# Performance work log

Measured on AMD Instinct MI355X. Metric: run time of the kernel, lower is better.

## Reference

```python
import jax, jax.numpy as jnp
import numpy as np

V, S, D, H, L = 32000, 2048, 768, 12, 6
HD = D // H
EPS = 1e-5


def _sinusoidal_pe(s, d):
    pos = np.arange(s)[:, None].astype(np.float32)
    div = np.exp(np.arange(0, d, 2).astype(np.float32) * (-np.log(10000.0) / d))
    pe = np.zeros((s, d), dtype=np.float32)
    pe[:, 0::2] = np.sin(pos * div)
    pe[:, 1::2] = np.cos(pos * div)
    return jnp.asarray(pe)


def setup_inputs() -> dict:
    key = jax.random.key(0)
    ks = jax.random.split(key, 16)
    std = 0.02
    tok_emb = jax.random.normal(ks[0], (V, D), jnp.float32) * std
    tok_emb = tok_emb.at[1].set(0.0)  # padding_idx=1
    pos_enc = _sinusoidal_pe(S, D)
    attn_w = jax.random.normal(ks[1], (L, 3 * D, D), jnp.float32) * std
    attn_b = jnp.zeros((L, 3 * D), jnp.float32)
    proj_std = 0.02 / np.sqrt(2 * 6)
    proj_w = jax.random.normal(ks[2], (L, D, D), jnp.float32) * proj_std
    proj_b = jnp.zeros((L, D), jnp.float32)
    ln1_g = jnp.ones((L, D), jnp.float32); ln1_b = jnp.zeros((L, D), jnp.float32)
    ln2_g = jnp.ones((L, D), jnp.float32); ln2_b = jnp.zeros((L, D), jnp.float32)
    fc1_w = jax.random.normal(ks[3], (L, 4 * D, D), jnp.float32) * std
    fc1_b = jnp.zeros((L, 4 * D), jnp.float32)
    fc2_w = jax.random.normal(ks[4], (L, D, 4 * D), jnp.float32) * std
    fc2_b = jnp.zeros((L, D), jnp.float32)
    dec_w = jax.random.normal(ks[5], (V, D), jnp.float32) * std
    idx = jax.random.randint(ks[6], (2, S), 0, V)
    return dict(idx=idx, tok_emb=tok_emb, pos_enc=pos_enc, attn_w=attn_w,
                attn_b=attn_b, proj_w=proj_w, proj_b=proj_b, ln1_g=ln1_g,
                ln1_b=ln1_b, ln2_g=ln2_g, ln2_b=ln2_b, fc1_w=fc1_w,
                fc1_b=fc1_b, fc2_w=fc2_w, fc2_b=fc2_b, dec_w=dec_w)


def _ln(x, g, b):
    mu = jnp.mean(x, -1, keepdims=True)
    var = jnp.mean(jnp.square(x - mu), -1, keepdims=True)
    return (x - mu) * jax.lax.rsqrt(var + EPS) * g + b


def _forward(idx, tok_emb, pos_enc, attn_w, attn_b, proj_w, proj_b,
             ln1_g, ln1_b, ln2_g, ln2_b, fc1_w, fc1_b, fc2_w, fc2_b, dec_w):
    b, s = idx.shape
    x = tok_emb[idx] + pos_enc[:s]  # [b,s,d]
    for l in range(L):
        h = _ln(x, ln1_g[l], ln1_b[l])
        qkv = h @ attn_w[l].T + attn_b[l]
        q, k, v = jnp.split(qkv, 3, axis=-1)
        q = q.reshape(b, s, H, HD).transpose(0, 2, 1, 3)
        k = k.reshape(b, s, H, HD).transpose(0, 2, 1, 3)
        v = v.reshape(b, s, H, HD).transpose(0, 2, 1, 3)
        att = jnp.einsum('bhqd,bhkd->bhqk', q, k) * (1.0 / np.sqrt(HD))
        att = jax.nn.softmax(att, axis=-1)  # no causal mask in source
        y = jnp.einsum('bhqk,bhkd->bhqd', att, v)
        y = y.transpose(0, 2, 1, 3).reshape(b, s, D)
        x = x + (y @ proj_w[l].T + proj_b[l])
        h = _ln(x, ln2_g[l], ln2_b[l])
        h = jax.nn.gelu(h @ fc1_w[l].T + fc1_b[l])
        x = x + (h @ fc2_w[l].T + fc2_b[l])
    return x @ dec_w.T  # [b,s,V]


def reference(idx, tok_emb, pos_enc, attn_w, attn_b, proj_w, proj_b,
              ln1_g, ln1_b, ln2_g, ln2_b, fc1_w, fc1_b, fc2_w, fc2_b, dec_w):
    return _forward(idx, tok_emb, pos_enc, attn_w, attn_b, proj_w, proj_b,
                    ln1_g, ln1_b, ln2_g, ln2_b, fc1_w, fc1_b, fc2_w, fc2_b, dec_w)
```

## Files before the change

### kernel.cpp

```cpp
#include <hip/hip_runtime.h>
#include <hip/hip_bf16.h>
#include <stdint.h>


typedef unsigned short u16;
typedef __attribute__((ext_vector_type(8))) __bf16 bf16x8;
typedef __attribute__((ext_vector_type(4))) float f32x4;
typedef __attribute__((ext_vector_type(4))) unsigned int u32x4;
typedef __attribute__((ext_vector_type(4))) unsigned short u16x4;
typedef __attribute__((ext_vector_type(8))) unsigned short u16x8;

#define MFMA16(a, b, c) __builtin_amdgcn_mfma_f32_16x16x32_bf16((a), (b), (c), 0, 0, 0)

__device__ __forceinline__ float b2f(u16 u) {
  union { unsigned int i; float f; } x; x.i = ((unsigned int)u) << 16; return x.f;
}
__device__ __forceinline__ u16 f2b(float f) {
  union { float f; unsigned int i; } x; x.f = f;
  unsigned int r = x.i + 0x7fffu + ((x.i >> 16) & 1u);
  return (u16)(r >> 16);
}
__device__ __forceinline__ float gelu_f(float v) {
  const float t = 0.7978845608028654f * (v + 0.044715f * v * v * v);
  const float e = __expf(-2.f * fabsf(t));
  float th = (1.f - e) / (1.f + e);
  th = (t < 0.f) ? -th : th;
  return 0.5f * v * (1.f + th);
}
__device__ __forceinline__ void lds16(u16* l, const u16* g) {
  __builtin_amdgcn_global_load_lds(
      (const __attribute__((address_space(1))) unsigned int*)g,
      (__attribute__((address_space(3))) unsigned int*)l, 16, 0, 0);
}

__global__ __launch_bounds__(256) void conv_bf16_kernel(
    const float* __restrict__ src, u16* __restrict__ dst, int n8) {
  int i = blockIdx.x * 256 + threadIdx.x;
  const int stride = gridDim.x * 256;
  for (; i < n8; i += stride) {
    const f32x4 a = *(const f32x4*)&src[(size_t)i * 8];
    const f32x4 b = *(const f32x4*)&src[(size_t)i * 8 + 4];
    u16x8 p;
#pragma unroll
    for (int j = 0; j < 4; ++j) { p[j] = f2b(a[j]); p[4 + j] = f2b(b[j]); }
    *(u16x8*)&dst[(size_t)i * 8] = p;
  }
}

__global__ __launch_bounds__(256) void embed_kernel(
    const int* __restrict__ idx, const float* __restrict__ tok,
    const float* __restrict__ pos, float* __restrict__ x) {
  const int t = blockIdx.x;
  const int s = t & 2047;
  const int tid = threadIdx.x;
  const size_t to = (size_t)idx[t] * 768;
  const size_t po = (size_t)s * 768;
  float* xr = x + (size_t)t * 768;
#pragma unroll
  for (int i = 0; i < 3; ++i) {
    const int d = tid + i * 256;
    xr[d] = tok[to + d] + pos[po + d];
  }
}

__global__ __launch_bounds__(256) void ln_kernel(
    const float* __restrict__ x, const float* __restrict__ g,
    const float* __restrict__ b, u16* __restrict__ out) {
  __shared__ float red[8];
  const int row = blockIdx.x;
  const int tid = threadIdx.x;
  const float* xr = x + (size_t)row * 768;
  const float v0 = xr[tid], v1 = xr[tid + 256], v2 = xr[tid + 512];
  float s = v0 + v1 + v2;
#pragma unroll
  for (int m = 1; m < 64; m <<= 1) s += __shfl_xor(s, m);
  const int w = tid >> 6, lane = tid & 63;
  if (lane == 0) red[w] = s;
  __syncthreads();
  const float mu = (red[0] + red[1] + red[2] + red[3]) * (1.f / 768.f);
  const float d0 = v0 - mu, d1 = v1 - mu, d2 = v2 - mu;
  float q = d0 * d0 + d1 * d1 + d2 * d2;
#pragma unroll
  for (int m = 1; m < 64; m <<= 1) q += __shfl_xor(q, m);
  if (lane == 0) red[4 + w] = q;
  __syncthreads();
  const float var = (red[4] + red[5] + red[6] + red[7]) * (1.f / 768.f);
  const float rs = rsqrtf(var + 1e-5f);
  u16* orow = out + (size_t)row * 768;
  orow[tid]       = f2b(d0 * rs * g[tid]       + b[tid]);
  orow[tid + 256] = f2b(d1 * rs * g[tid + 256] + b[tid + 256]);
  orow[tid + 512] = f2b(d2 * rs * g[tid + 512] + b[tid + 512]);
}

template <int MODE, int MFAST>
__global__ __launch_bounds__(256) void gemm_bb(
    const u16* __restrict__ A, const u16* __restrict__ B,
    const float* __restrict__ bias, u16* __restrict__ outb,
    float* __restrict__ outf, float* __restrict__ resid,
    u16* __restrict__ mirror, int N, int K) {
  __shared__ alignas(16) u16 As[128 * 64];
  __shared__ alignas(16) u16 Bs[128 * 64];
  const int tid = threadIdx.x;
  const int lane = tid & 63;
  const int w = tid >> 6;
  const int wr = (w >> 1) * 64;
  const int wc = (w & 1) * 64;
  const int fr = lane & 15;
  const int fg = lane >> 4;
  const int bn0 = (MFAST ? blockIdx.y : blockIdx.x) * 128;
  const int bm0 = (MFAST ? blockIdx.x : blockIdx.y) * 128;

  f32x4 acc[4][4] = {};
  const int srow = tid >> 3;

  for (int bk0 = 0; bk0 < K; bk0 += 64) {
    __syncthreads();
#pragma unroll
    for (int i = 0; i < 4; ++i) {
      const int row = i * 32 + srow;
      const int slot = (tid & 7) ^ (row & 7);
      lds16(&As[(size_t)(i * 256 + w * 64) * 8],
            &A[(size_t)(bm0 + row) * K + bk0 + slot * 8]);
      lds16(&Bs[(size_t)(i * 256 + w * 64) * 8],
            &B[(size_t)(bn0 + row) * K + bk0 + slot * 8]);
    }
    __syncthreads();
#pragma unroll
    for (int kk = 0; kk < 64; kk += 32) {
      bf16x8 af[4], bfv[4];
#pragma unroll
      for (int m = 0; m < 4; ++m) {
        const int row = wr + m * 16 + fr;
        const int slot = ((kk >> 3) + fg) ^ (row & 7);
        af[m] = *(const bf16x8*)&As[row * 64 + slot * 8];
      }
#pragma unroll
      for (int n = 0; n < 4; ++n) {
        const int row = wc + n * 16 + fr;
        const int slot = ((kk >> 3) + fg) ^ (row & 7);
        bfv[n] = *(const bf16x8*)&Bs[row * 64 + slot * 8];
      }
#pragma unroll
      for (int m = 0; m < 4; ++m)
#pragma unroll
        for (int n = 0; n < 4; ++n)
          acc[m][n] = MFMA16(af[m], bfv[n], acc[m][n]);
    }
  }

#pragma unroll
  for (int n = 0; n < 4; ++n) {
    const int col = bn0 + wc + n * 16 + fr;
    const float bv = bias ? bias[col] : 0.0f;
#pragma unroll
    for (int m = 0; m < 4; ++m) {
#pragma unroll
      for (int r = 0; r < 4; ++r) {
        const int row = bm0 + wr + m * 16 + fg * 4 + r;
        float v = acc[m][n][r] + bv;
        if (MODE == 1) v = gelu_f(v);
        const size_t off = (size_t)row * N + col;
        if (MODE == 2) {
          const float nv = resid[off] + v;
          resid[off] = nv;
          if (mirror) mirror[off] = f2b(nv);
        } else if (MODE == 3) {
          __builtin_nontemporal_store(v, &outf[off]);
        } else {
          outb[off] = f2b(v);
        }
      }
    }
  }
}

template <int MODE>
__global__ __launch_bounds__(256) void gemm_bt(
    const u16* __restrict__ A, const float* __restrict__ B,
    const float* __restrict__ bias, u16* __restrict__ outb,
    float* __restrict__ outf, float* __restrict__ resid,
    u16* __restrict__ mirror, int N, int K) {
  __shared__ alignas(16) u16 As[128 * 64];
  __shared__ alignas(16) u16 Bs[128 * 64];
  const int tid = threadIdx.x;
  const int lane = tid & 63;
  const int w = tid >> 6;
  const int wr = (w >> 1) * 64;
  const int wc = (w & 1) * 64;
  const int fr = lane & 15;
  const int fg = lane >> 4;
  const int bn0 = blockIdx.x * 128;
  const int bm0 = blockIdx.y * 128;

  f32x4 acc[4][4] = {};

  for (int bk0 = 0; bk0 < K; bk0 += 64) {
    __syncthreads();
#pragma unroll
    for (int i = 0; i < 4; ++i) {
      const int c = i * 256 + tid;
      const int row = c >> 3;
      const int e0 = (c & 7) * 8;
      *(u32x4*)&As[row * 64 + e0] =
          *(const u32x4*)&A[(size_t)(bm0 + row) * K + bk0 + e0];
    }
#pragma unroll
    for (int i = 0; i < 8; ++i) {
      const int c = i * 256 + tid;
      const int row = c >> 4;
      const int e0 = (c & 15) * 4;
      const f32x4 fv = *(const f32x4*)&B[(size_t)(bn0 + row) * K + bk0 + e0];
      u16x4 pv;
#pragma unroll
      for (int j = 0; j < 4; ++j) pv[j] = f2b(fv[j]);
      *(u16x4*)&Bs[row * 64 + e0] = pv;
    }
    __syncthreads();
#pragma unroll
    for (int kk = 0; kk < 64; kk += 32) {
      bf16x8 af[4], bfv[4];
#pragma unroll
      for (int m = 0; m < 4; ++m)
        af[m] = *(const bf16x8*)&As[(wr + m * 16 + fr) * 64 + kk + fg * 8];
#pragma unroll
      for (int n = 0; n < 4; ++n)
        bfv[n] = *(const bf16x8*)&Bs[(wc + n * 16 + fr) * 64 + kk + fg * 8];
#pragma unroll
      for (int m = 0; m < 4; ++m)
#pragma unroll
        for (int n = 0; n < 4; ++n)
          acc[m][n] = MFMA16(af[m], bfv[n], acc[m][n]);
    }
  }

#pragma unroll
  for (int n = 0; n < 4; ++n) {
    const int col = bn0 + wc + n * 16 + fr;
    const float bv = bias ? bias[col] : 0.0f;
#pragma unroll
    for (int m = 0; m < 4; ++m) {
#pragma unroll
      for (int r = 0; r < 4; ++r) {
        const int row = bm0 + wr + m * 16 + fg * 4 + r;
        float v = acc[m][n][r] + bv;
        if (MODE == 1) v = gelu_f(v);
        const size_t off = (size_t)row * N + col;
        if (MODE == 2) {
          const float nv = resid[off] + v;
          resid[off] = nv;
          if (mirror) mirror[off] = f2b(nv);
        } else if (MODE == 3) {
          __builtin_nontemporal_store(v, &outf[off]);
        } else {
          outb[off] = f2b(v);
        }
      }
    }
  }
}

__global__ __launch_bounds__(256) void vtrans_kernel(
    const u16* __restrict__ qkv, u16* __restrict__ vt) {
  __shared__ u16 tile[64][72];
  const int tid = threadIdx.x;
  const int s0 = blockIdx.x * 64;
  const int hh = blockIdx.y;
  const int bb = blockIdx.z;
  const size_t tb = (size_t)bb * 2048 * 2304;
#pragma unroll
  for (int i = 0; i < 2; ++i) {
    const int c = i * 256 + tid;
    const int sl = c >> 3;
    const int d0 = (c & 7) * 8;
    *(u16x8*)&tile[sl][d0] =
        *(const u16x8*)&qkv[tb + (size_t)(s0 + sl) * 2304 + 1536 + hh * 64 + d0];
  }
  __syncthreads();
  const size_t vtb = (size_t)((bb * 12 + hh) * 64) * 2048;
#pragma unroll
  for (int i = 0; i < 2; ++i) {
    const int c = i * 256 + tid;
    const int d = c >> 3;
    const int so = (c & 7) * 8;
    u16x8 p;
#pragma unroll
    for (int j = 0; j < 8; ++j) p[j] = tile[so + j][d];
    *(u16x8*)&vt[vtb + (size_t)d * 2048 + s0 + so] = p;
  }
}

__global__ __launch_bounds__(256) void attn_kernel(
    const u16* __restrict__ qkv, const u16* __restrict__ vt,
    u16* __restrict__ y) {
  __shared__ alignas(16) u16 Ks[2][64 * 64];
  __shared__ alignas(16) u16 VTs[2][64 * 64];
  __shared__ alignas(16) u16 Ps[4][16 * 64];
  const int tid = threadIdx.x;
  const int lane = tid & 63;
  const int w = tid >> 6;
  const int fr = lane & 15;
  const int fg = lane >> 4;
  const int hh = blockIdx.y;
  const int bb = blockIdx.z;
  const size_t tb = (size_t)bb * 2048 * 2304;
  const size_t vtb = (size_t)((bb * 12 + hh) * 64) * 2048;
  const int q0 = blockIdx.x * 64 + w * 16;

  const bf16x8 qf0 =
      *(const bf16x8*)&qkv[tb + (size_t)(q0 + fr) * 2304 + hh * 64 + fg * 8];
  const bf16x8 qf1 =
      *(const bf16x8*)&qkv[tb + (size_t)(q0 + fr) * 2304 + hh * 64 + 32 + fg * 8];

  f32x4 oacc[4] = {};
  float mrow[4] = {-INFINITY, -INFINITY, -INFINITY, -INFINITY};
  float lrow[4] = {0.f, 0.f, 0.f, 0.f};

  const int chunkrow = lane >> 3;
  const int chunkslot = lane & 7;

  auto stage = [&](int buf, int kt) {
#pragma unroll
    for (int i = 0; i < 2; ++i) {
      const int row = (i * 4 + w) * 8 + chunkrow;
      const int slot = chunkslot ^ (row & 7);
      lds16(&Ks[buf][(i * 4 + w) * 512],
            &qkv[tb + (size_t)(kt + row) * 2304 + 768 + hh * 64 + slot * 8]);
      lds16(&VTs[buf][(i * 4 + w) * 512],
            &vt[vtb + (size_t)row * 2048 + kt + slot * 8]);
    }
  };

  stage(0, 0);
  int cur = 0;
  for (int kt = 0; kt < 2048; kt += 64) {
    __syncthreads();
    if (kt + 64 < 2048) stage(cur ^ 1, kt + 64);

    f32x4 s[4] = {};
#pragma unroll
    for (int kb = 0; kb < 4; ++kb) {
      const int row = kb * 16 + fr;
      const int sl0 = (fg) ^ (row & 7);
      const int sl1 = (4 + fg) ^ (row & 7);
      const bf16x8 k0 = *(const bf16x8*)&Ks[cur][row * 64 + sl0 * 8];
      const bf16x8 k1 = *(const bf16x8*)&Ks[cur][row * 64 + sl1 * 8];
      s[kb] = MFMA16(qf0, k0, s[kb]);
      s[kb] = MFMA16(qf1, k1, s[kb]);
    }

    float alpha[4];
#pragma unroll
    for (int r = 0; r < 4; ++r) {
      float v[4];
#pragma unroll
      for (int kb = 0; kb < 4; ++kb) v[kb] = s[kb][r] * 0.125f;
      float mx = fmaxf(fmaxf(v[0], v[1]), fmaxf(v[2], v[3]));
      mx = fmaxf(mx, __shfl_xor(mx, 1));
      mx = fmaxf(mx, __shfl_xor(mx, 2));
      mx = fmaxf(mx, __shfl_xor(mx, 4));
      mx = fmaxf(mx, __shfl_xor(mx, 8));
      const float mn = fmaxf(mrow[r], mx);
      const float al = __expf(mrow[r] - mn);
      float p[4];
#pragma unroll
      for (int kb = 0; kb < 4; ++kb) p[kb] = __expf(v[kb] - mn);
      float ps = (p[0] + p[1]) + (p[2] + p[3]);
      ps += __shfl_xor(ps, 1);
      ps += __shfl_xor(ps, 2);
      ps += __shfl_xor(ps, 4);
      ps += __shfl_xor(ps, 8);
      lrow[r] = lrow[r] * al + ps;
      mrow[r] = mn;
      alpha[r] = al;
      const int q = fg * 4 + r;
#pragma unroll
      for (int kb = 0; kb < 4; ++kb) {
        const int kg = kb * 2 + (fr >> 3);
        Ps[w][q * 64 + ((kg ^ (q & 7)) << 3) + (fr & 7)] = f2b(p[kb]);
      }
    }
#pragma unroll
    for (int db = 0; db < 4; ++db)
#pragma unroll
      for (int r = 0; r < 4; ++r) oacc[db][r] *= alpha[r];

#pragma unroll
    for (int kh = 0; kh < 2; ++kh) {
      const bf16x8 pa =
          *(const bf16x8*)&Ps[w][fr * 64 + (((kh * 4 + fg) ^ (fr & 7)) << 3)];
#pragma unroll
      for (int db = 0; db < 4; ++db) {
        const int row = db * 16 + fr;
        const int slot = (kh * 4 + fg) ^ (row & 7);
        const bf16x8 vb = *(const bf16x8*)&VTs[cur][row * 64 + slot * 8];
        oacc[db] = MFMA16(pa, vb, oacc[db]);
      }
    }
    cur ^= 1;
  }

#pragma unroll
  for (int db = 0; db < 4; ++db) {
#pragma unroll
    for (int r = 0; r < 4; ++r) {
      const int row = q0 + fg * 4 + r;
      y[(size_t)(bb * 2048 + row) * 768 + hh * 64 + db * 16 + fr] =
          f2b(oacc[db][r] / lrow[r]);
    }
  }
}

extern "C" void kernel_launch(void* const* d_in, const int* in_sizes, int n_in,
                              void* d_out, int out_size, void* d_ws,
                              size_t ws_size, hipStream_t stream) {
  const int*   idx   = (const int*)d_in[0];
  const float* tok   = (const float*)d_in[1];
  const float* pos   = (const float*)d_in[2];
  const float* attnw = (const float*)d_in[3];
  const float* attnb = (const float*)d_in[4];
  const float* projw = (const float*)d_in[5];
  const float* projb = (const float*)d_in[6];
  const float* ln1g  = (const float*)d_in[7];
  const float* ln1b  = (const float*)d_in[8];
  const float* ln2g  = (const float*)d_in[9];
  const float* ln2b  = (const float*)d_in[10];
  const float* fc1w  = (const float*)d_in[11];
  const float* fc1b  = (const float*)d_in[12];
  const float* fc2w  = (const float*)d_in[13];
  const float* fc2b  = (const float*)d_in[14];
  const float* decw  = (const float*)d_in[15];

  char* ws = (char*)d_ws;
  float* x = (float*)(ws);
  u16* h   = (u16*)(ws + 12582912);
  u16* qkv = (u16*)(ws + 18874368);
  u16* y   = (u16*)(ws + 37748736);
  u16* h2  = (u16*)(ws + 18874368);
  u16* vt  = h;

  const size_t WB0 = 44040192;
  u16* attnw_b = (u16*)(ws + WB0);
  u16* projw_b = (u16*)(ws + WB0 + 21233664);
  u16* fc1w_b  = (u16*)(ws + WB0 + 28311552);
  u16* fc2w_b  = (u16*)(ws + WB0 + 56623104);
  u16* decw_b  = (u16*)(ws + WB0 + 84934656);
  const size_t NEED = WB0 + 84934656 + 49152000;

  embed_kernel<<<4096, 256, 0, stream>>>(idx, tok, pos, x);

  if (ws_size >= NEED) {
    conv_bf16_kernel<<<2048, 256, 0, stream>>>(attnw, attnw_b, 10616832 / 8);
    conv_bf16_kernel<<<2048, 256, 0, stream>>>(projw, projw_b, 3538944 / 8);
    conv_bf16_kernel<<<2048, 256, 0, stream>>>(fc1w, fc1w_b, 14155776 / 8);
    conv_bf16_kernel<<<2048, 256, 0, stream>>>(fc2w, fc2w_b, 14155776 / 8);
    conv_bf16_kernel<<<2048, 256, 0, stream>>>(decw, decw_b, 24576000 / 8);

    for (int l = 0; l < 6; ++l) {
      ln_kernel<<<4096, 256, 0, stream>>>(x, ln1g + l * 768, ln1b + l * 768, h);
      gemm_bb<0, 0><<<dim3(18, 32), 256, 0, stream>>>(
          h, attnw_b + (size_t)l * 2304 * 768, attnb + l * 2304, qkv, nullptr,
          nullptr, nullptr, 2304, 768);
      vtrans_kernel<<<dim3(32, 12, 2), 256, 0, stream>>>(qkv, vt);
      attn_kernel<<<dim3(32, 12, 2), 256, 0, stream>>>(qkv, vt, y);
      gemm_bb<2, 0><<<dim3(6, 32), 256, 0, stream>>>(
          y, projw_b + (size_t)l * 768 * 768, projb + l * 768, nullptr, nullptr,
          x, nullptr, 768, 768);
      ln_kernel<<<4096, 256, 0, stream>>>(x, ln2g + l * 768, ln2b + l * 768, h);
      gemm_bb<1, 0><<<dim3(24, 32), 256, 0, stream>>>(
          h, fc1w_b + (size_t)l * 3072 * 768, fc1b + l * 3072, h2, nullptr,
          nullptr, nullptr, 3072, 768);
      gemm_bb<2, 0><<<dim3(6, 32), 256, 0, stream>>>(
          h2, fc2w_b + (size_t)l * 768 * 3072, fc2b + l * 768, nullptr, nullptr,
          x, (l == 5) ? h : nullptr, 768, 3072);
    }
    gemm_bb<3, 1><<<dim3(32, 250), 256, 0, stream>>>(
        h, decw_b, nullptr, nullptr, (float*)d_out, nullptr, nullptr, 32000,
        768);
  } else {
    for (int l = 0; l < 6; ++l) {
      ln_kernel<<<4096, 256, 0, stream>>>(x, ln1g + l * 768, ln1b + l * 768, h);
      gemm_bt<0><<<dim3(18, 32), 256, 0, stream>>>(
          h, attnw + (size_t)l * 2304 * 768, attnb + l * 2304, qkv, nullptr,
          nullptr, nullptr, 2304, 768);
      vtrans_kernel<<<dim3(32, 12, 2), 256, 0, stream>>>(qkv, vt);
      attn_kernel<<<dim3(32, 12, 2), 256, 0, stream>>>(qkv, vt, y);
      gemm_bt<2><<<dim3(6, 32), 256, 0, stream>>>(
          y, projw + (size_t)l * 768 * 768, projb + l * 768, nullptr, nullptr,
          x, nullptr, 768, 768);
      ln_kernel<<<4096, 256, 0, stream>>>(x, ln2g + l * 768, ln2b + l * 768, h);
      gemm_bt<1><<<dim3(24, 32), 256, 0, stream>>>(
          h, fc1w + (size_t)l * 3072 * 768, fc1b + l * 3072, h2, nullptr,
          nullptr, nullptr, 3072, 768);
      gemm_bt<2><<<dim3(6, 32), 256, 0, stream>>>(
          h2, fc2w + (size_t)l * 768 * 3072, fc2b + l * 768, nullptr, nullptr,
          x, (l == 5) ? h : nullptr, 768, 3072);
    }
    gemm_bt<3><<<dim3(250, 32), 256, 0, stream>>>(
        h, decw, nullptr, nullptr, (float*)d_out, nullptr, nullptr, 32000, 768);
  }
}
```

Baseline: 2.009 ms.

## Double-buffer GEMM LDS tiles, use one wave per row in layernorm, skip attention rescale

The bf16 GEMM now uses two LDS buffers for A and B and prefetches the next K tile before computing the current one. This overlaps global loads with MFMA work, at the cost of doubling the shared-memory footprint to 64KB per block, which may lower occupancy. LayerNorm now gives one wavefront to each row with vectorized float4 loads and no block-level sync, launching 1024 blocks. In the attention kernel, the row-max shuffle reduction and the rescaling of the output accumulator are skipped when no lane's max exceeds the running max.

```diff
diff --git a/kernel.cpp b/kernel.cpp
--- a/kernel.cpp
+++ b/kernel.cpp
@@ -66,30 +66,41 @@
 __global__ __launch_bounds__(256) void ln_kernel(
     const float* __restrict__ x, const float* __restrict__ g,
     const float* __restrict__ b, u16* __restrict__ out) {
-  __shared__ float red[8];
-  const int row = blockIdx.x;
-  const int tid = threadIdx.x;
+  const int w = threadIdx.x >> 6, lane = threadIdx.x & 63;
+  const int row = blockIdx.x * 4 + w;
   const float* xr = x + (size_t)row * 768;
-  const float v0 = xr[tid], v1 = xr[tid + 256], v2 = xr[tid + 512];
-  float s = v0 + v1 + v2;
+  f32x4 v[3];
+#pragma unroll
+  for (int i = 0; i < 3; ++i) v[i] = *(const f32x4*)&xr[i * 256 + lane * 4];
+  float s = 0.f;
+#pragma unroll
+  for (int i = 0; i < 3; ++i)
+#pragma unroll
+    for (int j = 0; j < 4; ++j) s += v[i][j];
 #pragma unroll
   for (int m = 1; m < 64; m <<= 1) s += __shfl_xor(s, m);
-  const int w = tid >> 6, lane = tid & 63;
-  if (lane == 0) red[w] = s;
-  __syncthreads();
-  const float mu = (red[0] + red[1] + red[2] + red[3]) * (1.f / 768.f);
-  const float d0 = v0 - mu, d1 = v1 - mu, d2 = v2 - mu;
-  float q = d0 * d0 + d1 * d1 + d2 * d2;
+  const float mu = s * (1.f / 768.f);
+  float q = 0.f;
+#pragma unroll
+  for (int i = 0; i < 3; ++i)
+#pragma unroll
+    for (int j = 0; j < 4; ++j) {
+      const float d = v[i][j] - mu;
+      q += d * d;
+    }
 #pragma unroll
   for (int m = 1; m < 64; m <<= 1) q += __shfl_xor(q, m);
-  if (lane == 0) red[4 + w] = q;
-  __syncthreads();
-  const float var = (red[4] + red[5] + red[6] + red[7]) * (1.f / 768.f);
-  const float rs = rsqrtf(var + 1e-5f);
+  const float rs = rsqrtf(q * (1.f / 768.f) + 1e-5f);
   u16* orow = out + (size_t)row * 768;
-  orow[tid]       = f2b(d0 * rs * g[tid]       + b[tid]);
-  orow[tid + 256] = f2b(d1 * rs * g[tid + 256] + b[tid + 256]);
-  orow[tid + 512] = f2b(d2 * rs * g[tid + 512] + b[tid + 512]);
+#pragma unroll
+  for (int i = 0; i < 3; ++i) {
+    const f32x4 gg = *(const f32x4*)&g[i * 256 + lane * 4];
+    const f32x4 bb = *(const f32x4*)&b[i * 256 + lane * 4];
+    u16x4 o;
+#pragma unroll
+    for (int j = 0; j < 4; ++j) o[j] = f2b((v[i][j] - mu) * rs * gg[j] + bb[j]);
+    *(u16x4*)&orow[i * 256 + lane * 4] = o;
+  }
 }
 
 template <int MODE, int MFAST>
@@ -98,8 +109,8 @@
     const float* __restrict__ bias, u16* __restrict__ outb,
     float* __restrict__ outf, float* __restrict__ resid,
     u16* __restrict__ mirror, int N, int K) {
-  __shared__ alignas(16) u16 As[128 * 64];
-  __shared__ alignas(16) u16 Bs[128 * 64];
+  __shared__ alignas(16) u16 As[2][128 * 64];
+  __shared__ alignas(16) u16 Bs[2][128 * 64];
   const int tid = threadIdx.x;
   const int lane = tid & 63;
   const int w = tid >> 6;
@@ -109,22 +120,27 @@
   const int fg = lane >> 4;
   const int bn0 = (MFAST ? blockIdx.y : blockIdx.x) * 128;
   const int bm0 = (MFAST ? blockIdx.x : blockIdx.y) * 128;
+  const int srow = tid >> 3;
 
   f32x4 acc[4][4] = {};
-  const int srow = tid >> 3;
-
-  for (int bk0 = 0; bk0 < K; bk0 += 64) {
-    __syncthreads();
+
+  auto stage = [&](int buf, int bk0) {
 #pragma unroll
     for (int i = 0; i < 4; ++i) {
       const int row = i * 32 + srow;
       const int slot = (tid & 7) ^ (row & 7);
-      lds16(&As[(size_t)(i * 256 + w * 64) * 8],
+      lds16(&As[buf][(i * 256 + w * 64) * 8],
             &A[(size_t)(bm0 + row) * K + bk0 + slot * 8]);
-      lds16(&Bs[(size_t)(i * 256 + w * 64) * 8],
+      lds16(&Bs[buf][(i * 256 + w * 64) * 8],
             &B[(size_t)(bn0 + row) * K + bk0 + slot * 8]);
     }
+  };
+
+  stage(0, 0);
+  int cur = 0;
+  for (int bk0 = 0; bk0 < K; bk0 += 64) {
     __syncthreads();
+    if (bk0 + 64 < K) stage(cur ^ 1, bk0 + 64);
 #pragma unroll
     for (int kk = 0; kk < 64; kk += 32) {
       bf16x8 af[4], bfv[4];
@@ -132,13 +148,13 @@
       for (int m = 0; m < 4; ++m) {
         const int row = wr + m * 16 + fr;
         const int slot = ((kk >> 3) + fg) ^ (row & 7);
-        af[m] = *(const bf16x8*)&As[row * 64 + slot * 8];
+        af[m] = *(const bf16x8*)&As[cur][row * 64 + slot * 8];
       }
 #pragma unroll
       for (int n = 0; n < 4; ++n) {
         const int row = wc + n * 16 + fr;
         const int slot = ((kk >> 3) + fg) ^ (row & 7);
-        bfv[n] = *(const bf16x8*)&Bs[row * 64 + slot * 8];
+        bfv[n] = *(const bf16x8*)&Bs[cur][row * 64 + slot * 8];
       }
 #pragma unroll
       for (int m = 0; m < 4; ++m)
@@ -146,6 +162,7 @@
         for (int n = 0; n < 4; ++n)
           acc[m][n] = MFMA16(af[m], bfv[n], acc[m][n]);
     }
+    cur ^= 1;
   }
 
 #pragma unroll
@@ -349,18 +366,26 @@
     }
 
     float alpha[4];
+    bool anyresc = false;
 #pragma unroll
     for (int r = 0; r < 4; ++r) {
       float v[4];
 #pragma unroll
       for (int kb = 0; kb < 4; ++kb) v[kb] = s[kb][r] * 0.125f;
       float mx = fmaxf(fmaxf(v[0], v[1]), fmaxf(v[2], v[3]));
-      mx = fmaxf(mx, __shfl_xor(mx, 1));
-      mx = fmaxf(mx, __shfl_xor(mx, 2));
-      mx = fmaxf(mx, __shfl_xor(mx, 4));
-      mx = fmaxf(mx, __shfl_xor(mx, 8));
-      const float mn = fmaxf(mrow[r], mx);
-      const float al = __expf(mrow[r] - mn);
+      float mn = mrow[r];
+      if (__all(mx <= mn)) {
+        alpha[r] = 1.f;
+      } else {
+        mx = fmaxf(mx, __shfl_xor(mx, 1));
+        mx = fmaxf(mx, __shfl_xor(mx, 2));
+        mx = fmaxf(mx, __shfl_xor(mx, 4));
+        mx = fmaxf(mx, __shfl_xor(mx, 8));
+        mn = fmaxf(mrow[r], mx);
+        alpha[r] = __expf(mrow[r] - mn);
+        mrow[r] = mn;
+        anyresc = true;
+      }
       float p[4];
 #pragma unroll
       for (int kb = 0; kb < 4; ++kb) p[kb] = __expf(v[kb] - mn);
@@ -369,9 +394,7 @@
       ps += __shfl_xor(ps, 2);
       ps += __shfl_xor(ps, 4);
       ps += __shfl_xor(ps, 8);
-      lrow[r] = lrow[r] * al + ps;
-      mrow[r] = mn;
-      alpha[r] = al;
+      lrow[r] = lrow[r] * alpha[r] + ps;
       const int q = fg * 4 + r;
 #pragma unroll
       for (int kb = 0; kb < 4; ++kb) {
@@ -379,10 +402,12 @@
         Ps[w][q * 64 + ((kg ^ (q & 7)) << 3) + (fr & 7)] = f2b(p[kb]);
       }
     }
-#pragma unroll
-    for (int db = 0; db < 4; ++db)
-#pragma unroll
-      for (int r = 0; r < 4; ++r) oacc[db][r] *= alpha[r];
+    if (anyresc) {
+#pragma unroll
+      for (int db = 0; db < 4; ++db)
+#pragma unroll
+        for (int r = 0; r < 4; ++r) oacc[db][r] *= alpha[r];
+    }
 
 #pragma unroll
     for (int kh = 0; kh < 2; ++kh) {
@@ -456,7 +481,7 @@
     conv_bf16_kernel<<<2048, 256, 0, stream>>>(decw, decw_b, 24576000 / 8);
 
     for (int l = 0; l < 6; ++l) {
-      ln_kernel<<<4096, 256, 0, stream>>>(x, ln1g + l * 768, ln1b + l * 768, h);
+      ln_kernel<<<1024, 256, 0, stream>>>(x, ln1g + l * 768, ln1b + l * 768, h);
       gemm_bb<0, 0><<<dim3(18, 32), 256, 0, stream>>>(
           h, attnw_b + (size_t)l * 2304 * 768, attnb + l * 2304, qkv, nullptr,
           nullptr, nullptr, 2304, 768);
@@ -465,7 +490,7 @@
       gemm_bb<2, 0><<<dim3(6, 32), 256, 0, stream>>>(
           y, projw_b + (size_t)l * 768 * 768, projb + l * 768, nullptr, nullptr,
           x, nullptr, 768, 768);
-      ln_kernel<<<4096, 256, 0, stream>>>(x, ln2g + l * 768, ln2b + l * 768, h);
+      ln_kernel<<<1024, 256, 0, stream>>>(x, ln2g + l * 768, ln2b + l * 768, h);
       gemm_bb<1, 0><<<dim3(24, 32), 256, 0, stream>>>(
           h, fc1w_b + (size_t)l * 3072 * 768, fc1b + l * 3072, h2, nullptr,
           nullptr, nullptr, 3072, 768);
@@ -478,7 +503,7 @@
         768);
   } else {
     for (int l = 0; l < 6; ++l) {
-      ln_kernel<<<4096, 256, 0, stream>>>(x, ln1g + l * 768, ln1b + l * 768, h);
+      ln_kernel<<<1024, 256, 0, stream>>>(x, ln1g + l * 768, ln1b + l * 768, h);
       gemm_bt<0><<<dim3(18, 32), 256, 0, stream>>>(
           h, attnw + (size_t)l * 2304 * 768, attnb + l * 2304, qkv, nullptr,
           nullptr, nullptr, 2304, 768);
@@ -487,7 +512,7 @@
       gemm_bt<2><<<dim3(6, 32), 256, 0, stream>>>(
           y, projw + (size_t)l * 768 * 768, projb + l * 768, nullptr, nullptr,
           x, nullptr, 768, 768);
-      ln_kernel<<<4096, 256, 0, stream>>>(x, ln2g + l * 768, ln2b + l * 768, h);
+      ln_kernel<<<1024, 256, 0, stream>>>(x, ln2g + l * 768, ln2b + l * 768, h);
       gemm_bt<1><<<dim3(24, 32), 256, 0, stream>>>(
           h, fc1w + (size_t)l * 3072 * 768, fc1b + l * 3072, h2, nullptr,
           nullptr, nullptr, 3072, 768);
```

Measured after the change: 2.014 ms. Within noise of the previous version (+0.3%).
